# Kernel optimization log

Hardware: AMD Instinct MI355X
Metric: run time of the kernel (lower is better)

## Reference

```python
import jax, jax.numpy as jnp
import numpy as np

MAX_DISP = 40   # init kwarg max_disp
STRIDE_2 = 1    # init kwarg stride_2


def setup_inputs() -> dict:
    key = jax.random.key(0)
    k1, k2 = jax.random.split(key)
    B, C, H, W = 8, 128, 160, 320
    x_1 = jax.random.normal(k1, (B, C, H, W), dtype=jnp.float32)
    x_2 = jax.random.normal(k2, (B, C, H, W), dtype=jnp.float32)
    return {"x_1": x_1, "x_2": x_2}


def reference(x_1, x_2):
    # x_1, x_2: [B, C, H, W]
    pad = MAX_DISP * 2
    W = x_1.shape[3]
    # left-pad x_2 along width, matching F.pad(x_2, (pad, 0, 0, 0))
    x2p = jnp.pad(x_2, ((0, 0), (0, 0), (0, 0), (pad, 0)))
    # one [B,H,W] correlation map per displacement (small fixed set of 81 shifts)
    outs = [
        jnp.sum(x_1 * jax.lax.dynamic_slice_in_dim(x2p, d, W, axis=3), axis=1)
        for d in range(0, pad + 1, STRIDE_2)
    ]
    return jnp.stack(outs, axis=1)  # [B, D, H, W], D = 2*max_disp//stride + 1
```

## Files before the change

### kernel.cpp

```cpp
#include <hip/hip_runtime.h>


#define CB 8
#define CC 128
#define CH 160
#define CW 320
#define CD 81
#define CPAD 80
#define TW 64
#define NTHR 256
#define BROWS 144
#define NTILE 576
#define KC 64
#define ROWP 72
#define EP 65
#define HW (CH*CW)

typedef __attribute__((ext_vector_type(8))) short short8;
typedef __attribute__((ext_vector_type(4))) float f32x4;

__device__ __forceinline__ unsigned cvt_pk(float lo, float hi) {
    unsigned r;
    asm("v_cvt_pk_bf16_f32 %0, %1, %2" : "=v"(r) : "v"(lo), "v"(hi));
    return r;
}

__global__ __launch_bounds__(NTHR, 6) void corr1d_mfma(
    const float* __restrict__ x1,
    const float* __restrict__ x2,
    float* __restrict__ out)
{
    __shared__ __align__(16) char smem[21072];
    unsigned short* lB = reinterpret_cast<unsigned short*>(smem);
    float* eO = reinterpret_cast<float*>(smem);

    const int tid = threadIdx.x;
    const int bid = blockIdx.x;

    const int v  = (bid & 7) * 800 + (bid >> 3);
    const int g  = v / 5;
    const int wt = v - 5 * g;
    const int b  = g / CH;
    const int h  = g - b * CH;
    const int w0 = wt * TW;

    const int lane = tid & 63;
    const int s    = tid >> 6;
    const int n    = lane & 15;
    const int q    = lane >> 4;

    const float* x1p = x1 + ((size_t)b * CC * CH + (size_t)h) * CW;
    const float* x2p = x2 + ((size_t)b * CC * CH + (size_t)h) * CW;

    short8 aF[4];
    {
        const float* ap = x1p + (size_t)(8 * q) * HW + (w0 + 16 * s + n);
#pragma unroll
        for (int kf = 0; kf < 4; kf++) {
            const float* p = ap + (size_t)(32 * kf) * HW;
            float f0 = p[0];
            float f1 = p[(size_t)1 * HW];
            float f2 = p[(size_t)2 * HW];
            float f3 = p[(size_t)3 * HW];
            float f4 = p[(size_t)4 * HW];
            float f5 = p[(size_t)5 * HW];
            float f6 = p[(size_t)6 * HW];
            float f7 = p[(size_t)7 * HW];
            union { unsigned u[4]; short8 v8; } cv;
            cv.u[0] = cvt_pk(f0, f1);
            cv.u[1] = cvt_pk(f2, f3);
            cv.u[2] = cvt_pk(f4, f5);
            cv.u[3] = cvt_pk(f6, f7);
            aF[kf] = cv.v8;
        }
    }

    f32x4 acc[6];
#pragma unroll
    for (int t = 0; t < 6; t++) acc[t] = (f32x4){0.f, 0.f, 0.f, 0.f};

#pragma unroll
    for (int half = 0; half < 2; half++) {
        const int c0 = half * KC;
        if (half) __syncthreads();

#pragma unroll
        for (int j = 0; j < 3; j++) {
            const int i = tid + j * NTHR;
            if (i < NTILE) {
                const int cq = i & 15;
                const int rt = i >> 4;
                const int kl = cq << 2;
                const int gw = w0 - CPAD + (rt << 2);
                float4 v0, v1, v2, v3;
                if (gw >= 0) {
                    const float* p = x2p + (size_t)(c0 + kl) * HW + gw;
                    v0 = *(const float4*)(p);
                    v1 = *(const float4*)(p + (size_t)1 * HW);
                    v2 = *(const float4*)(p + (size_t)2 * HW);
                    v3 = *(const float4*)(p + (size_t)3 * HW);
                } else {
                    v0 = v1 = v2 = v3 = make_float4(0.f, 0.f, 0.f, 0.f);
                }
                unsigned short* dst = &lB[(rt << 2) * ROWP + kl];
                *(uint2*)(dst + 0 * ROWP) = make_uint2(cvt_pk(v0.x, v1.x), cvt_pk(v2.x, v3.x));
                *(uint2*)(dst + 1 * ROWP) = make_uint2(cvt_pk(v0.y, v1.y), cvt_pk(v2.y, v3.y));
                *(uint2*)(dst + 2 * ROWP) = make_uint2(cvt_pk(v0.z, v1.z), cvt_pk(v2.z, v3.z));
                *(uint2*)(dst + 3 * ROWP) = make_uint2(cvt_pk(v0.w, v1.w), cvt_pk(v2.w, v3.w));
            }
        }
        __syncthreads();

#pragma unroll
        for (int ko = 0; ko < 2; ko++) {
            const short8 av = aF[half * 2 + ko];
            const unsigned short* bb = &lB[(size_t)n * ROWP + ko * 32 + 8 * q];
#pragma unroll
            for (int t = 0; t < 6; t++) {
                short8 bv = *(const short8*)(bb + (size_t)(16 * (s + t)) * ROWP);
                acc[t] = __builtin_amdgcn_mfma_f32_16x16x32_bf16(av, bv, acc[t], 0, 0, 0);
            }
        }
    }

    __syncthreads();

#pragma unroll
    for (int t = 0; t < 6; t++) {
#pragma unroll
        for (int r = 0; r < 4; r++) {
            int m = 4 * q + r;
            int d = 16 * t + n - m;
            if (d >= 0 && d <= CPAD)
                eO[d * EP + 16 * s + m] = acc[t][r];
        }
    }
    __syncthreads();

    float* op = out + ((size_t)b * CD * CH + (size_t)h) * CW + w0;
#pragma unroll
    for (int j = 0; j < 21; j++) {
        int idx = tid + j * NTHR;
        if (idx < CD * TW) {
            int d = idx >> 6;
            int w = idx & 63;
            op[(size_t)d * HW + w] = eO[d * EP + w];
        }
    }
}

extern "C" void kernel_launch(void* const* d_in, const int* in_sizes, int n_in,
                              void* d_out, int out_size, void* d_ws, size_t ws_size,
                              hipStream_t stream) {
    const float* x1 = (const float*)d_in[0];
    const float* x2 = (const float*)d_in[1];
    float* out = (float*)d_out;
    dim3 grid(CB * CH * 5);
    dim3 block(NTHR);
    corr1d_mfma<<<grid, block, 0, stream>>>(x1, x2, out);
}
```

Baseline: 472.0 us.

## Stage full channel depth in LDS at once and vectorize output stores

Both channel halves of x2 are now loaded into a wider LDS tile (ROWP 136) before a single barrier, so there is one load phase followed by 24 MFMAs instead of two load/compute phases. This removes a barrier and lets all x2 global loads be in flight together. The x1 loads are issued as a batch before conversion, and the epilogue writes float4 instead of scalar floats, with the LDS pitch padded to 68 for alignment. The cost is roughly double the LDS per block, so launch bounds drop from 6 to 4 blocks and occupancy falls.

After: 469.0 us. About the same (-0.6%).

```diff
diff --git a/kernel.cpp b/kernel.cpp
--- a/kernel.cpp
+++ b/kernel.cpp
@@ -10,10 +10,8 @@
 #define TW 64
 #define NTHR 256
 #define BROWS 144
-#define NTILE 576
-#define KC 64
-#define ROWP 72
-#define EP 65
+#define ROWP 136
+#define EP 68
 #define HW (CH*CW)
 
 typedef __attribute__((ext_vector_type(8))) short short8;
@@ -25,12 +23,12 @@
     return r;
 }
 
-__global__ __launch_bounds__(NTHR, 6) void corr1d_mfma(
+__global__ __launch_bounds__(NTHR, 4) void corr1d_mfma(
     const float* __restrict__ x1,
     const float* __restrict__ x2,
     float* __restrict__ out)
 {
-    __shared__ __align__(16) char smem[21072];
+    __shared__ __align__(16) char smem[39168];
     unsigned short* lB = reinterpret_cast<unsigned short*>(smem);
     float* eO = reinterpret_cast<float*>(smem);
 
@@ -52,27 +50,23 @@
     const float* x1p = x1 + ((size_t)b * CC * CH + (size_t)h) * CW;
     const float* x2p = x2 + ((size_t)b * CC * CH + (size_t)h) * CW;
 
-    short8 aF[4];
+    float araw[32];
     {
         const float* ap = x1p + (size_t)(8 * q) * HW + (w0 + 16 * s + n);
 #pragma unroll
-        for (int kf = 0; kf < 4; kf++) {
-            const float* p = ap + (size_t)(32 * kf) * HW;
-            float f0 = p[0];
-            float f1 = p[(size_t)1 * HW];
-            float f2 = p[(size_t)2 * HW];
-            float f3 = p[(size_t)3 * HW];
-            float f4 = p[(size_t)4 * HW];
-            float f5 = p[(size_t)5 * HW];
-            float f6 = p[(size_t)6 * HW];
-            float f7 = p[(size_t)7 * HW];
-            union { unsigned u[4]; short8 v8; } cv;
-            cv.u[0] = cvt_pk(f0, f1);
-            cv.u[1] = cvt_pk(f2, f3);
-            cv.u[2] = cvt_pk(f4, f5);
-            cv.u[3] = cvt_pk(f6, f7);
-            aF[kf] = cv.v8;
-        }
+        for (int kf = 0; kf < 4; kf++)
+#pragma unroll
+            for (int j = 0; j < 8; j++)
+                araw[kf * 8 + j] = ap[(size_t)(32 * kf + j) * HW];
+    }
+    short8 aF[4];
+#pragma unroll
+    for (int kf = 0; kf < 4; kf++) {
+        union { unsigned u[4]; short8 v8; } cv;
+#pragma unroll
+        for (int p = 0; p < 4; p++)
+            cv.u[p] = cvt_pk(araw[kf * 8 + 2 * p], araw[kf * 8 + 2 * p + 1]);
+        aF[kf] = cv.v8;
     }
 
     f32x4 acc[6];
@@ -80,14 +74,12 @@
     for (int t = 0; t < 6; t++) acc[t] = (f32x4){0.f, 0.f, 0.f, 0.f};
 
 #pragma unroll
-    for (int half = 0; half < 2; half++) {
-        const int c0 = half * KC;
-        if (half) __syncthreads();
-
+    for (int khalf = 0; khalf < 2; khalf++) {
+        const int c0 = khalf * 64;
 #pragma unroll
         for (int j = 0; j < 3; j++) {
             const int i = tid + j * NTHR;
-            if (i < NTILE) {
+            if (i < 576) {
                 const int cq = i & 15;
                 const int rt = i >> 4;
                 const int kl = cq << 2;
@@ -102,24 +94,24 @@
                 } else {
                     v0 = v1 = v2 = v3 = make_float4(0.f, 0.f, 0.f, 0.f);
                 }
-                unsigned short* dst = &lB[(rt << 2) * ROWP + kl];
+                unsigned short* dst = &lB[(rt << 2) * ROWP + c0 + kl];
                 *(uint2*)(dst + 0 * ROWP) = make_uint2(cvt_pk(v0.x, v1.x), cvt_pk(v2.x, v3.x));
                 *(uint2*)(dst + 1 * ROWP) = make_uint2(cvt_pk(v0.y, v1.y), cvt_pk(v2.y, v3.y));
                 *(uint2*)(dst + 2 * ROWP) = make_uint2(cvt_pk(v0.z, v1.z), cvt_pk(v2.z, v3.z));
                 *(uint2*)(dst + 3 * ROWP) = make_uint2(cvt_pk(v0.w, v1.w), cvt_pk(v2.w, v3.w));
             }
         }
-        __syncthreads();
+    }
+    __syncthreads();
 
 #pragma unroll
-        for (int ko = 0; ko < 2; ko++) {
-            const short8 av = aF[half * 2 + ko];
-            const unsigned short* bb = &lB[(size_t)n * ROWP + ko * 32 + 8 * q];
+    for (int ko = 0; ko < 4; ko++) {
+        const short8 av = aF[ko];
+        const unsigned short* bb = &lB[(size_t)n * ROWP + ko * 32 + 8 * q];
 #pragma unroll
-            for (int t = 0; t < 6; t++) {
-                short8 bv = *(const short8*)(bb + (size_t)(16 * (s + t)) * ROWP);
-                acc[t] = __builtin_amdgcn_mfma_f32_16x16x32_bf16(av, bv, acc[t], 0, 0, 0);
-            }
+        for (int t = 0; t < 6; t++) {
+            short8 bv = *(const short8*)(bb + (size_t)(16 * (s + t)) * ROWP);
+            acc[t] = __builtin_amdgcn_mfma_f32_16x16x32_bf16(av, bv, acc[t], 0, 0, 0);
         }
     }
 
@@ -139,12 +131,13 @@
 
     float* op = out + ((size_t)b * CD * CH + (size_t)h) * CW + w0;
 #pragma unroll
-    for (int j = 0; j < 21; j++) {
+    for (int j = 0; j < 6; j++) {
         int idx = tid + j * NTHR;
-        if (idx < CD * TW) {
-            int d = idx >> 6;
-            int w = idx & 63;
-            op[(size_t)d * HW + w] = eO[d * EP + w];
+        if (idx < CD * 16) {
+            int d  = idx >> 4;
+            int wq = idx & 15;
+            *(float4*)(op + (size_t)d * HW + 4 * wq) =
+                *(const float4*)(&eO[d * EP + 4 * wq]);
         }
     }
 }
```
